# Kernel optimization log

Measured on AMD Instinct MI355X. Metric: run time of the kernel, lower is better.

The kernel has to match this reference:

```python
import jax, jax.numpy as jnp
import numpy as np

VOCAB = 32000
D = 1024
H = 8
S = 2048
DFF = 3 * D
EPS = 1e-5


def setup_inputs() -> dict:
    key = jax.random.key(0)
    ks = jax.random.split(key, 12)
    sc = 0.02
    return {
        "tokens": jax.random.randint(ks[0], (S,), 0, VOCAB, dtype=jnp.int32),
        "emb": jax.random.normal(ks[1], (VOCAB, D), jnp.float32) * sc,
        "Wq": jax.random.normal(ks[2], (H, D, D), jnp.float32) * sc,
        "bq": jnp.zeros((H, D), jnp.float32),
        "Wk": jax.random.normal(ks[3], (H, D, D), jnp.float32) * sc,
        "bk": jnp.zeros((H, D), jnp.float32),
        "Wv": jax.random.normal(ks[4], (H, D, D), jnp.float32) * sc,
        "bv": jnp.zeros((H, D), jnp.float32),
        "W1": jax.random.normal(ks[5], (D, DFF), jnp.float32) * sc,
        "b1": jnp.zeros((DFF,), jnp.float32),
        "W2": jax.random.normal(ks[6], (DFF, D), jnp.float32) * sc,
        "b2": jnp.zeros((D,), jnp.float32),
    }


def _positional_encoding(seq_len, d_model, dtype):
    pos = jnp.arange(seq_len, dtype=dtype)[:, None]        # [S,1]
    i = jnp.arange(d_model)                                 # [D]
    angle = pos / jnp.power(10000.0, (2 * (i // 2)).astype(dtype) / d_model)
    return jnp.where(i % 2 == 0, jnp.sin(angle), jnp.cos(angle))  # [S,D]


def reference(tokens, emb, Wq, bq, Wk, bk, Wv, bv, W1, b1, W2, b2):
    # embedding + sinusoidal positional encoding
    x = emb[tokens] + _positional_encoding(tokens.shape[0], D, emb.dtype)  # [S,D]

    # multi-head attention: sum of H full-dimension scaled-dot-product heads
    q = jnp.einsum('sd,hde->hse', x, Wq) + bq[:, None, :]   # [H,S,D]
    k = jnp.einsum('sd,hde->hse', x, Wk) + bk[:, None, :]
    v = jnp.einsum('sd,hde->hse', x, Wv) + bv[:, None, :]
    scores = jnp.einsum('hse,hte->hst', q, k) / jnp.sqrt(jnp.asarray(D, x.dtype))
    attn = jax.nn.softmax(scores, axis=-1)                  # [H,S,S]
    mha = jnp.einsum('hst,hte->hse', attn, v).sum(axis=0)   # [S,D]

    # residual + layer_norm over the whole tensor (normalized_shape = X.size())
    z = mha + x
    zn = (z - z.mean()) * jax.lax.rsqrt(z.var() + EPS)

    # feed-forward: relu(D->3D) then 3D->D
    h = jax.nn.relu(zn @ W1 + b1)
    return h @ W2 + b2
```

## Files before the change

### kernel.cpp

```cpp
#include <hip/hip_runtime.h>
#include <hip/hip_bf16.h>

#define D 1024
#define H 8
#define S 2048
#define DFF 3072
#define HD 8192
#define EPS 1e-5f

typedef __attribute__((ext_vector_type(8))) short short8;
typedef __attribute__((ext_vector_type(4))) float float4v;
typedef __attribute__((ext_vector_type(8))) unsigned short u16x8;

#define F_OUT_BF16 1
#define F_RELU     4
#define F_BIAS_COL 8
#define F_BIAS_ROW 16

__device__ __forceinline__ void async16(void* lds, const void* g) {
    __builtin_amdgcn_global_load_lds(
        (const __attribute__((address_space(1))) unsigned int*)g,
        (__attribute__((address_space(3))) unsigned int*)lds, 16, 0, 0);
}

__global__ __launch_bounds__(256) void gemm_bt(
    const __hip_bfloat16* __restrict__ A,
    const __hip_bfloat16* __restrict__ Bt,
    void* __restrict__ Cout,
    const float* __restrict__ bias,
    int M, int N, int K,
    int lda, int ldb, int ldc,
    long sA, long sB, long sC, int sBias,
    int kSplit, long sAz, long sBz, long sCz,
    int nkb, long sAk, long sBk,
    float alpha, int flags)
{
    __shared__ __align__(16) __hip_bfloat16 As[128 * 32];
    __shared__ __align__(16) __hip_bfloat16 Bs[128 * 32];

    const int z  = blockIdx.z;
    const int z2 = z / kSplit;
    const int kz = z - z2 * kSplit;
    A  += (long)z2 * sA + (long)kz * sAz;
    Bt += (long)z2 * sB + (long)kz * sBz;
    const float* bp = bias ? bias + (long)z2 * sBias : nullptr;

    const int nn = gridDim.x, nm = gridDim.y;
    const int tot = nm * nn;
    const int pid = blockIdx.y * nn + blockIdx.x;
    const int lin = (pid & 7) * (tot >> 3) + (pid >> 3);
    const int bandh = nm << 2;
    const int band = lin / bandh;
    const int rr = lin - band * bandh;
    const int m0 = (rr >> 2) * 128;
    const int n0 = (band * 4 + (rr & 3)) * 128;

    const int t    = threadIdx.x;
    const int wave = t >> 6;
    const int lane = t & 63;
    const int lr   = lane & 15;
    const int lq   = lane >> 4;
    const int lqx  = lq ^ ((lr >> 1) & 3);
    const int wm   = (wave >> 1) * 64;
    const int wn   = (wave & 1) * 64;

    const int srow = t >> 2;
    const int skc  = (t & 3) ^ ((t >> 3) & 3);
    const __hip_bfloat16* Ap1 = A  + (long)(m0 + srow) * lda + skc * 8;
    const __hip_bfloat16* Ap2 = Ap1 + 64L * lda;
    const __hip_bfloat16* Bp1 = Bt + (long)(n0 + srow) * ldb + skc * 8;
    const __hip_bfloat16* Bp2 = Bp1 + 64L * ldb;
    uint4* dA1 = (uint4*)As + t;
    uint4* dA2 = (uint4*)As + t + 256;
    uint4* dB1 = (uint4*)Bs + t;
    uint4* dB2 = (uint4*)Bs + t + 256;

    float4v acc[4][4];
    const float4v vzero = {0.f, 0.f, 0.f, 0.f};
    #pragma unroll
    for (int i = 0; i < 4; i++)
        #pragma unroll
        for (int j = 0; j < 4; j++) acc[i][j] = vzero;

    for (int kb = 0; kb < nkb; kb++) {
        for (int k0 = 0; k0 < K; k0 += 32) {
            __syncthreads();
            async16(dA1, Ap1);
            async16(dA2, Ap2);
            async16(dB1, Bp1);
            async16(dB2, Bp2);
            Ap1 += 32; Ap2 += 32; Bp1 += 32; Bp2 += 32;
            __syncthreads();

            short8 af[4], bf[4];
            #pragma unroll
            for (int i = 0; i < 4; i++)
                af[i] = *(const short8*)&As[(wm + i * 16 + lr) * 32 + lqx * 8];
            #pragma unroll
            for (int i = 0; i < 4; i++)
                bf[i] = *(const short8*)&Bs[(wn + i * 16 + lr) * 32 + lqx * 8];

            #pragma unroll
            for (int mi = 0; mi < 4; mi++)
                #pragma unroll
                for (int ni = 0; ni < 4; ni++)
                    acc[mi][ni] = __builtin_amdgcn_mfma_f32_16x16x32_bf16(
                        af[mi], bf[ni], acc[mi][ni], 0, 0, 0);
        }
        Ap1 += sAk - K; Ap2 += sAk - K;
        Bp1 += sBk - K; Bp2 += sBk - K;
    }

    __hip_bfloat16* Cb = (__hip_bfloat16*)Cout + (long)z2 * sC + (long)kz * sCz;
    float*          Cf = (float*)Cout          + (long)z2 * sC + (long)kz * sCz;

    #pragma unroll
    for (int mi = 0; mi < 4; mi++) {
        #pragma unroll
        for (int r = 0; r < 4; r++) {
            const int row = m0 + wm + mi * 16 + lq * 4 + r;
            const float brow = (bp && (flags & F_BIAS_ROW)) ? bp[row] : 0.f;
            #pragma unroll
            for (int ni = 0; ni < 4; ni++) {
                const int col = n0 + wn + ni * 16 + lr;
                float v = acc[mi][ni][r] * alpha + brow;
                if (bp && (flags & F_BIAS_COL)) v += bp[col];
                if (flags & F_RELU) v = fmaxf(v, 0.f);
                const long idx = (long)row * ldc + col;
                if (flags & F_OUT_BF16) Cb[idx] = __float2bfloat16(v);
                else                    Cf[idx] = v;
            }
        }
    }
}

__global__ __launch_bounds__(256) void transpose_cast(
    const float* __restrict__ in, __hip_bfloat16* __restrict__ out, int R, int C)
{
    __shared__ float tile[32][33];
    const long boff = (long)blockIdx.z * R * C;
    const int c0 = blockIdx.x * 32, r0 = blockIdx.y * 32;
    const int tx = threadIdx.x & 31, ty = threadIdx.x >> 5;
    #pragma unroll
    for (int i = ty; i < 32; i += 8)
        tile[i][tx] = in[boff + (long)(r0 + i) * C + c0 + tx];
    __syncthreads();
    #pragma unroll
    for (int i = ty; i < 32; i += 8)
        out[boff + (long)(c0 + i) * R + r0 + tx] = __float2bfloat16(tile[tx][i]);
}

__global__ __launch_bounds__(256) void concat_bias(
    const float* __restrict__ a, const float* __restrict__ b,
    float* __restrict__ o)
{
    const int i = blockIdx.x * 256 + threadIdx.x;
    o[i] = (i < HD) ? a[i] : b[i - HD];
}

__global__ __launch_bounds__(256) void embed_pos(
    const int* __restrict__ tokens, const float* __restrict__ emb,
    float* __restrict__ xf, __hip_bfloat16* __restrict__ xb)
{
    const int s = blockIdx.x;
    const int tok = tokens[s];
    for (int d = threadIdx.x; d < D; d += 256) {
        const float e = emb[(long)tok * D + d];
        const float expo = (float)((d >> 1) << 1) / (float)D;
        const float angle = (float)s * powf(10000.f, -expo);
        const float pe = (d & 1) ? cosf(angle) : sinf(angle);
        const float v = e + pe;
        xf[(long)s * D + d] = v;
        xb[(long)s * D + d] = __float2bfloat16(v);
    }
}

__global__ __launch_bounds__(256) void softmax_rows(__hip_bfloat16* __restrict__ Sc)
{
    __hip_bfloat16* p = Sc + (long)blockIdx.x * S;
    const int t = threadIdx.x;
    const int wave = t >> 6, lane = t & 63;
    __shared__ float wred[4], wsum[4];

    u16x8 u = ((const u16x8*)p)[t];
    float v[8];
    float mx = -1e30f;
    #pragma unroll
    for (int j = 0; j < 8; j++) {
        const unsigned int b = ((unsigned int)u[j]) << 16;
        v[j] = __builtin_bit_cast(float, b);
        mx = fmaxf(mx, v[j]);
    }
    #pragma unroll
    for (int off = 32; off; off >>= 1) mx = fmaxf(mx, __shfl_down(mx, off));
    if (lane == 0) wred[wave] = mx;
    __syncthreads();
    mx = fmaxf(fmaxf(wred[0], wred[1]), fmaxf(wred[2], wred[3]));

    float sum = 0.f;
    #pragma unroll
    for (int j = 0; j < 8; j++) { v[j] = expf(v[j] - mx); sum += v[j]; }
    #pragma unroll
    for (int off = 32; off; off >>= 1) sum += __shfl_down(sum, off);
    if (lane == 0) wsum[wave] = sum;
    __syncthreads();
    sum = wsum[0] + wsum[1] + wsum[2] + wsum[3];

    const float inv = 1.f / sum;
    u16x8 o;
    #pragma unroll
    for (int j = 0; j < 8; j++) {
        const __hip_bfloat16 h = __float2bfloat16(v[j] * inv);
        o[j] = __builtin_bit_cast(unsigned short, h);
    }
    ((u16x8*)p)[t] = o;
}

__global__ __launch_bounds__(256) void attn_reduce(
    const float* __restrict__ pvp, const float* __restrict__ xf,
    float* __restrict__ z, float* __restrict__ stats)
{
    const long SD = (long)S * D;
    const long i0 = (long)blockIdx.x * 2048 + threadIdx.x;
    float s = 0.f, s2 = 0.f;
    #pragma unroll
    for (int j = 0; j < 8; j++) {
        const long i = i0 + j * 256;
        const float v = pvp[i] + pvp[i + SD] + pvp[i + 2 * SD] + pvp[i + 3 * SD]
                        + xf[i];
        z[i] = v;
        s += v; s2 += v * v;
    }
    #pragma unroll
    for (int off = 32; off; off >>= 1) { s += __shfl_down(s, off); s2 += __shfl_down(s2, off); }
    const int wave = threadIdx.x >> 6, lane = threadIdx.x & 63;
    __shared__ float ws1[4], ws2[4];
    if (lane == 0) { ws1[wave] = s; ws2[wave] = s2; }
    __syncthreads();
    if (threadIdx.x == 0) {
        atomicAdd(&stats[0], ws1[0] + ws1[1] + ws1[2] + ws1[3]);
        atomicAdd(&stats[1], ws2[0] + ws2[1] + ws2[2] + ws2[3]);
    }
}

__global__ __launch_bounds__(256) void ln_cast(
    const float* __restrict__ z, const float* __restrict__ stats,
    __hip_bfloat16* __restrict__ zn)
{
    const float invN = 1.f / (float)(S * D);
    const float mean = stats[0] * invN;
    const float var  = stats[1] * invN - mean * mean;
    const float rs   = rsqrtf(var + EPS);
    const long i0 = (long)blockIdx.x * 2048 + threadIdx.x;
    #pragma unroll
    for (int j = 0; j < 8; j++) {
        const long i = i0 + j * 256;
        zn[i] = __float2bfloat16((z[i] - mean) * rs);
    }
}

__global__ __launch_bounds__(256) void ff2_reduce(
    const float* __restrict__ ffp, const float* __restrict__ b2,
    float* __restrict__ out)
{
    const long SD = (long)S * D;
    const long i0 = (long)blockIdx.x * 2048 + threadIdx.x;
    #pragma unroll
    for (int j = 0; j < 8; j++) {
        const long i = i0 + j * 256;
        out[i] = ffp[i] + ffp[i + SD] + ffp[i + 2 * SD] + ffp[i + 3 * SD]
                 + b2[i & (D - 1)];
    }
}

extern "C" void kernel_launch(void* const* d_in, const int* in_sizes, int n_in,
                              void* d_out, int out_size, void* d_ws, size_t ws_size,
                              hipStream_t stream)
{
    const int*   tokens = (const int*)  d_in[0];
    const float* emb    = (const float*)d_in[1];
    const float* Wq     = (const float*)d_in[2];
    const float* bq     = (const float*)d_in[3];
    const float* Wk     = (const float*)d_in[4];
    const float* bk     = (const float*)d_in[5];
    const float* Wv     = (const float*)d_in[6];
    const float* bv     = (const float*)d_in[7];
    const float* W1     = (const float*)d_in[8];
    const float* b1     = (const float*)d_in[9];
    const float* W2     = (const float*)d_in[10];
    const float* b2     = (const float*)d_in[11];
    float* out = (float*)d_out;

    char* w = (char*)d_ws;
    const long MB = 1 << 20;
    __hip_bfloat16* XB   = (__hip_bfloat16*)(w + 0 * MB);
    float*          XF   = (float*)(w + 4 * MB);
    __hip_bfloat16* W1T  = (__hip_bfloat16*)(w + 12 * MB);
    __hip_bfloat16* W2T  = (__hip_bfloat16*)(w + 18 * MB);
    __hip_bfloat16* WQT  = (__hip_bfloat16*)(w + 24 * MB);
    __hip_bfloat16* WKT  = (__hip_bfloat16*)(w + 40 * MB);
    __hip_bfloat16* SC   = (__hip_bfloat16*)(w + 24 * MB);
    __hip_bfloat16* QK   = (__hip_bfloat16*)(w + 88 * MB);
    __hip_bfloat16* VT   = (__hip_bfloat16*)(w + 88 * MB);
    float*          PVP  = (float*)(w + 120 * MB);
    __hip_bfloat16* WVT  = (__hip_bfloat16*)(w + 152 * MB);
    float*          Z    = (float*)(w + 152 * MB);
    __hip_bfloat16* ZN   = (__hip_bfloat16*)(w + 0 * MB);
    __hip_bfloat16* FFH  = (__hip_bfloat16*)(w + 24 * MB);
    float*          FF2P = (float*)(w + 40 * MB);
    float*          STATS = (float*)(w + 168 * MB);
    float*          BQK   = (float*)(w + 168 * MB + 4096);

    hipMemsetAsync(STATS, 0, 256, stream);

    embed_pos<<<S, 256, 0, stream>>>(tokens, emb, XF, XB);

    transpose_cast<<<dim3(32, 32, H), 256, 0, stream>>>(Wq, WQT, D, D);
    transpose_cast<<<dim3(32, 32, H), 256, 0, stream>>>(Wk, WKT, D, D);
    transpose_cast<<<dim3(32, 32, H), 256, 0, stream>>>(Wv, WVT, D, D);
    transpose_cast<<<dim3(96, 32, 1), 256, 0, stream>>>(W1, W1T, D, DFF);
    transpose_cast<<<dim3(32, 96, 1), 256, 0, stream>>>(W2, W2T, DFF, D);
    concat_bias<<<2 * HD / 256, 256, 0, stream>>>(bq, bk, BQK);

    const float inv_sqrt_d = 0.03125f;

    gemm_bt<<<dim3(2 * HD / 128, S / 128), 256, 0, stream>>>(
        XB, WQT, QK, BQK, S, 2 * HD, D, D, D, 2 * HD,
        0, 0, 0, 0,  1, 0, 0, 0,  1, 0, 0,  1.f, F_OUT_BF16 | F_BIAS_COL);

    gemm_bt<<<dim3(S / 128, S / 128, H), 256, 0, stream>>>(
        QK, QK + HD, SC, (const float*)nullptr, S, S, D, 2 * HD, 2 * HD, S,
        D, D, (long)S * S, 0,  1, 0, 0, 0,  1, 0, 0,  inv_sqrt_d, F_OUT_BF16);

    softmax_rows<<<H * S, 256, 0, stream>>>(SC);

    gemm_bt<<<dim3(S / 128, D / 128, H), 256, 0, stream>>>(
        WVT, XB, VT, bv, D, S, D, D, D, S,
        (long)D * D, 0, (long)D * S, D,  1, 0, 0, 0,  1, 0, 0,  1.f,
        F_OUT_BF16 | F_BIAS_ROW);

    gemm_bt<<<dim3(D / 128, S / 128, 4), 256, 0, stream>>>(
        SC, VT, PVP, (const float*)nullptr, S, D, S, S, S, D,
        0, 0, 0, 0,
        4, (long)2 * S * S, (long)2 * D * S, (long)S * D,
        2, (long)S * S, (long)D * S,
        1.f, 0);

    attn_reduce<<<(S * D) / 2048, 256, 0, stream>>>(PVP, XF, Z, STATS);
    ln_cast<<<(S * D) / 2048, 256, 0, stream>>>(Z, STATS, ZN);

    gemm_bt<<<dim3(DFF / 128, S / 128), 256, 0, stream>>>(
        ZN, W1T, FFH, b1, S, DFF, D, D, D, DFF,
        0, 0, 0, 0,  1, 0, 0, 0,  1, 0, 0,  1.f,
        F_OUT_BF16 | F_BIAS_COL | F_RELU);

    gemm_bt<<<dim3(D / 128, S / 128, 4), 256, 0, stream>>>(
        FFH, W2T, FF2P, (const float*)nullptr, S, D, DFF / 4, DFF, DFF, D,
        0, 0, 0, 0,
        4, (long)DFF / 4, (long)DFF / 4, (long)S * D,
        1, 0, 0,
        1.f, 0);

    ff2_reduce<<<(S * D) / 2048, 256, 0, stream>>>(FF2P, b2, out);
}
```

Measured before the change: 772.5 us.

## Double GEMM K-tile to 64 and store per-head PV partials in bf16

The shared GEMM kernel now stages a 64-wide K slice per iteration instead of 32, with a wider XOR swizzle. This halves the number of barrier pairs per K and issues two MFMA rounds per load. Separately, the PV GEMM now writes one bf16 partial per head (8 slices) instead of 4 fp32 partials that each summed two heads over a K loop. The reduction kernel is vectorized to read those bf16 slices, which cuts write traffic but adds bf16 rounding to each per-head partial before summation. LDS use doubles to 32 KB per block, which may lower occupancy.

```diff
diff --git a/kernel.cpp b/kernel.cpp
--- a/kernel.cpp
+++ b/kernel.cpp
@@ -35,8 +35,8 @@
     int nkb, long sAk, long sBk,
     float alpha, int flags)
 {
-    __shared__ __align__(16) __hip_bfloat16 As[128 * 32];
-    __shared__ __align__(16) __hip_bfloat16 Bs[128 * 32];
+    __shared__ __align__(16) __hip_bfloat16 As[128 * 64];
+    __shared__ __align__(16) __hip_bfloat16 Bs[128 * 64];
 
     const int z  = blockIdx.z;
     const int z2 = z / kSplit;
@@ -60,20 +60,23 @@
     const int lane = t & 63;
     const int lr   = lane & 15;
     const int lq   = lane >> 4;
-    const int lqx  = lq ^ ((lr >> 1) & 3);
+    const int lqx0 = lq ^ (lr & 7);
     const int wm   = (wave >> 1) * 64;
     const int wn   = (wave & 1) * 64;
 
-    const int srow = t >> 2;
-    const int skc  = (t & 3) ^ ((t >> 3) & 3);
-    const __hip_bfloat16* Ap1 = A  + (long)(m0 + srow) * lda + skc * 8;
-    const __hip_bfloat16* Ap2 = Ap1 + 64L * lda;
-    const __hip_bfloat16* Bp1 = Bt + (long)(n0 + srow) * ldb + skc * 8;
-    const __hip_bfloat16* Bp2 = Bp1 + 64L * ldb;
-    uint4* dA1 = (uint4*)As + t;
-    uint4* dA2 = (uint4*)As + t + 256;
-    uint4* dB1 = (uint4*)Bs + t;
-    uint4* dB2 = (uint4*)Bs + t + 256;
+    const int r0 = t >> 3;
+    const int kc = (t & 7) ^ ((t >> 3) & 7);
+    const __hip_bfloat16* Ap[4];
+    const __hip_bfloat16* Bp[4];
+    uint4* dA[4];
+    uint4* dB[4];
+    #pragma unroll
+    for (int i = 0; i < 4; i++) {
+        Ap[i] = A  + (long)(m0 + r0 + 32 * i) * lda + kc * 8;
+        Bp[i] = Bt + (long)(n0 + r0 + 32 * i) * ldb + kc * 8;
+        dA[i] = (uint4*)As + t + 256 * i;
+        dB[i] = (uint4*)Bs + t + 256 * i;
+    }
 
     float4v acc[4][4];
     const float4v vzero = {0.f, 0.f, 0.f, 0.f};
@@ -83,23 +86,35 @@
         for (int j = 0; j < 4; j++) acc[i][j] = vzero;
 
     for (int kb = 0; kb < nkb; kb++) {
-        for (int k0 = 0; k0 < K; k0 += 32) {
+        for (int k0 = 0; k0 < K; k0 += 64) {
             __syncthreads();
-            async16(dA1, Ap1);
-            async16(dA2, Ap2);
-            async16(dB1, Bp1);
-            async16(dB2, Bp2);
-            Ap1 += 32; Ap2 += 32; Bp1 += 32; Bp2 += 32;
+            #pragma unroll
+            for (int i = 0; i < 4; i++) async16(dA[i], Ap[i]);
+            #pragma unroll
+            for (int i = 0; i < 4; i++) async16(dB[i], Bp[i]);
+            #pragma unroll
+            for (int i = 0; i < 4; i++) { Ap[i] += 64; Bp[i] += 64; }
             __syncthreads();
 
             short8 af[4], bf[4];
             #pragma unroll
             for (int i = 0; i < 4; i++)
-                af[i] = *(const short8*)&As[(wm + i * 16 + lr) * 32 + lqx * 8];
+                af[i] = *(const short8*)&As[(wm + i * 16 + lr) * 64 + lqx0 * 8];
             #pragma unroll
             for (int i = 0; i < 4; i++)
-                bf[i] = *(const short8*)&Bs[(wn + i * 16 + lr) * 32 + lqx * 8];
-
+                bf[i] = *(const short8*)&Bs[(wn + i * 16 + lr) * 64 + lqx0 * 8];
+            #pragma unroll
+            for (int mi = 0; mi < 4; mi++)
+                #pragma unroll
+                for (int ni = 0; ni < 4; ni++)
+                    acc[mi][ni] = __builtin_amdgcn_mfma_f32_16x16x32_bf16(
+                        af[mi], bf[ni], acc[mi][ni], 0, 0, 0);
+            #pragma unroll
+            for (int i = 0; i < 4; i++)
+                af[i] = *(const short8*)&As[(wm + i * 16 + lr) * 64 + (lqx0 ^ 4) * 8];
+            #pragma unroll
+            for (int i = 0; i < 4; i++)
+                bf[i] = *(const short8*)&Bs[(wn + i * 16 + lr) * 64 + (lqx0 ^ 4) * 8];
             #pragma unroll
             for (int mi = 0; mi < 4; mi++)
                 #pragma unroll
@@ -107,8 +122,11 @@
                     acc[mi][ni] = __builtin_amdgcn_mfma_f32_16x16x32_bf16(
                         af[mi], bf[ni], acc[mi][ni], 0, 0, 0);
         }
-        Ap1 += sAk - K; Ap2 += sAk - K;
-        Bp1 += sBk - K; Bp2 += sBk - K;
+        #pragma unroll
+        for (int i = 0; i < 4; i++) {
+            Ap[i] += sAk - K;
+            Bp[i] += sBk - K;
+        }
     }
 
     __hip_bfloat16* Cb = (__hip_bfloat16*)Cout + (long)z2 * sC + (long)kz * sCz;
@@ -217,20 +235,41 @@
 }
 
 __global__ __launch_bounds__(256) void attn_reduce(
-    const float* __restrict__ pvp, const float* __restrict__ xf,
+    const __hip_bfloat16* __restrict__ pvb, const float* __restrict__ xf,
     float* __restrict__ z, float* __restrict__ stats)
 {
     const long SD = (long)S * D;
-    const long i0 = (long)blockIdx.x * 2048 + threadIdx.x;
+    const long i0 = (long)blockIdx.x * 2048 + threadIdx.x * 8;
     float s = 0.f, s2 = 0.f;
-    #pragma unroll
-    for (int j = 0; j < 8; j++) {
-        const long i = i0 + j * 256;
-        const float v = pvp[i] + pvp[i + SD] + pvp[i + 2 * SD] + pvp[i + 3 * SD]
-                        + xf[i];
-        z[i] = v;
-        s += v; s2 += v * v;
-    }
+    float v[8];
+    {
+        const float4* x4 = (const float4*)(xf + i0);
+        #pragma unroll
+        for (int j = 0; j < 2; j++) {
+            const float4 x = x4[j];
+            v[j * 4 + 0] = x.x; v[j * 4 + 1] = x.y;
+            v[j * 4 + 2] = x.z; v[j * 4 + 3] = x.w;
+        }
+    }
+    #pragma unroll
+    for (int sl = 0; sl < H; sl++) {
+        const u16x8 u = *(const u16x8*)(pvb + sl * SD + i0);
+        #pragma unroll
+        for (int j = 0; j < 8; j++) {
+            const unsigned int b = ((unsigned int)u[j]) << 16;
+            v[j] += __builtin_bit_cast(float, b);
+        }
+    }
+    float4* z4 = (float4*)(z + i0);
+    #pragma unroll
+    for (int j = 0; j < 2; j++) {
+        float4 o;
+        o.x = v[j * 4 + 0]; o.y = v[j * 4 + 1];
+        o.z = v[j * 4 + 2]; o.w = v[j * 4 + 3];
+        z4[j] = o;
+    }
+    #pragma unroll
+    for (int j = 0; j < 8; j++) { s += v[j]; s2 += v[j] * v[j]; }
     #pragma unroll
     for (int off = 32; off; off >>= 1) { s += __shfl_down(s, off); s2 += __shfl_down(s2, off); }
     const int wave = threadIdx.x >> 6, lane = threadIdx.x & 63;
@@ -302,7 +341,7 @@
     __hip_bfloat16* SC   = (__hip_bfloat16*)(w + 24 * MB);
     __hip_bfloat16* QK   = (__hip_bfloat16*)(w + 88 * MB);
     __hip_bfloat16* VT   = (__hip_bfloat16*)(w + 88 * MB);
-    float*          PVP  = (float*)(w + 120 * MB);
+    __hip_bfloat16* PVB  = (__hip_bfloat16*)(w + 120 * MB);
     __hip_bfloat16* WVT  = (__hip_bfloat16*)(w + 152 * MB);
     float*          Z    = (float*)(w + 152 * MB);
     __hip_bfloat16* ZN   = (__hip_bfloat16*)(w + 0 * MB);
@@ -339,14 +378,14 @@
         (long)D * D, 0, (long)D * S, D,  1, 0, 0, 0,  1, 0, 0,  1.f,
         F_OUT_BF16 | F_BIAS_ROW);
 
-    gemm_bt<<<dim3(D / 128, S / 128, 4), 256, 0, stream>>>(
-        SC, VT, PVP, (const float*)nullptr, S, D, S, S, S, D,
+    gemm_bt<<<dim3(D / 128, S / 128, 8), 256, 0, stream>>>(
+        SC, VT, PVB, (const float*)nullptr, S, D, S, S, S, D,
         0, 0, 0, 0,
-        4, (long)2 * S * S, (long)2 * D * S, (long)S * D,
-        2, (long)S * S, (long)D * S,
-        1.f, 0);
-
-    attn_reduce<<<(S * D) / 2048, 256, 0, stream>>>(PVP, XF, Z, STATS);
+        8, (long)S * S, (long)D * S, (long)S * D,
+        1, 0, 0,
+        1.f, F_OUT_BF16);
+
+    attn_reduce<<<(S * D) / 2048, 256, 0, stream>>>(PVB, XF, Z, STATS);
     ln_cast<<<(S * D) / 2048, 256, 0, stream>>>(Z, STATS, ZN);
 
     gemm_bt<<<dim3(DFF / 128, S / 128), 256, 0, stream>>>(
```

Measured after the change: 716.8 us. 1.08x faster.
